# Performance work log

Hardware: AMD Instinct MI355X
Metric: run time of the kernel (lower is better)

Reference implementation:

```python
import jax, jax.numpy as jnp
import numpy as np


def _conv(x, w, b=None, pad=0):
    # x: [B,C,H,W], w: [O,I,kh,kw]
    y = jax.lax.conv_general_dilated(
        x, w, window_strides=(1, 1), padding=[(pad, pad), (pad, pad)],
        dimension_numbers=('NCHW', 'OIHW', 'NCHW'))
    if b is not None:
        y = y + b[None, :, None, None]
    return y


def _resb(x, w1, w2):
    h = _conv(x, w1, pad=1)
    h = jax.nn.leaky_relu(h, 0.1)
    h = _conv(h, w2, pad=1)
    return h + x


def setup_inputs() -> dict:
    key = jax.random.key(0)
    ks = jax.random.split(key, 16)
    B, C, H, W, K = 2, 64, 128, 256, 16
    s = 0.05
    return {
        'x_left': jax.random.normal(ks[0], (B, C, H, W), jnp.float32),
        'x_right': jax.random.normal(ks[1], (B, C, H, W), jnp.float32),
        'xxs': jax.random.randint(ks[2], (B, H * W, K), 0, H, jnp.int32),
        'yys': jax.random.randint(ks[3], (B, H * W, K), 0, W, jnp.int32),
        'is_training': 0,
        'rb_w1': jax.random.normal(ks[4], (C, C, 3, 3), jnp.float32) * s,
        'rb_w2': jax.random.normal(ks[5], (C, C, 3, 3), jnp.float32) * s,
        'b1_w': jax.random.normal(ks[6], (C, C, 1, 1), jnp.float32) * s,
        'b1_b': jax.random.normal(ks[7], (C,), jnp.float32) * s,
        'b2_w': jax.random.normal(ks[8], (C, C, 1, 1), jnp.float32) * s,
        'b2_b': jax.random.normal(ks[9], (C,), jnp.float32) * s,
        'b3_w': jax.random.normal(ks[10], (C, C, 1, 1), jnp.float32) * s,
        'b3_b': jax.random.normal(ks[11], (C,), jnp.float32) * s,
        'fus_w': jax.random.normal(ks[12], (C, 2 * C, 1, 1), jnp.float32) * s,
        'fus_b': jax.random.normal(ks[13], (C,), jnp.float32) * s,
    }


def reference(x_left, x_right, xxs, yys, is_training,
              rb_w1, rb_w2, b1_w, b1_b, b2_w, b2_b, b3_w, b3_b, fus_w, fus_b):
    B, C, H, W = x_left.shape
    HW = H * W
    K = xxs.shape[-1]

    buf_l = _resb(x_left, rb_w1, rb_w2)
    buf_r = _resb(x_right, rb_w1, rb_w2)

    Q = _conv(buf_l, b1_w, b1_b)   # [B,C,H,W]
    S = _conv(buf_r, b2_w, b2_b)
    R = _conv(buf_r, b3_w, b3_b)

    # per-pixel gather: S[b,:,Pos_x,Pos_y] -> flat index into H*W
    flat = (xxs.astype(jnp.int32) * W + yys.astype(jnp.int32)).reshape(B, HW * K)  # [B,HW*K]
    Sf = S.reshape(B, C, HW)
    Rf = R.reshape(B, C, HW)
    Key = jnp.take_along_axis(Sf, flat[:, None, :], axis=2).reshape(B, C, HW, K)
    Val = jnp.take_along_axis(Rf, flat[:, None, :], axis=2).reshape(B, C, HW, K)

    Qv = Q.transpose(0, 2, 3, 1).reshape(B, HW, C)           # [B,HW,C]
    score = jnp.einsum('bpc,bcpk->bpk', Qv, Key)             # [B,HW,K]
    M = jax.nn.softmax(score, axis=-1)                       # [B,HW,K]
    buf = jnp.einsum('bpk,bckp->bpc', M, Val.transpose(0, 1, 3, 2))  # [B,HW,C]
    buf = buf.reshape(B, H, W, C).transpose(0, 3, 1, 2)      # [B,C,H,W]

    out = _conv(jnp.concatenate([buf, x_left], axis=1), fus_w, fus_b)
    M_right_to_left = M[:, :, None, :]                       # [B,HW,1,K] as in torch
    if is_training == 1:
        return out
    return (out, M_right_to_left)
```

## Files before the change

kernel.cpp:

```cpp
#include <hip/hip_runtime.h>

#define HH 128
#define WW 256
#define CH 64
#define HWP (HH * WW)

typedef __attribute__((ext_vector_type(8))) __bf16 bf16x8;
typedef __attribute__((ext_vector_type(16))) float float16;

__device__ __forceinline__ unsigned short f2bf(float f) {
    unsigned u = __float_as_uint(f);
    u += 0x7fffu + ((u >> 16) & 1u);
    return (unsigned short)(u >> 16);
}
__device__ __forceinline__ float bf2f(unsigned short u) {
    return __uint_as_float((unsigned)u << 16);
}

__global__ __launch_bounds__(256) void prep_w_k(
    const float* __restrict__ w1, const float* __restrict__ w2,
    const float* __restrict__ b1w, const float* __restrict__ b2w,
    const float* __restrict__ b3w, const float* __restrict__ fusw,
    unsigned short* __restrict__ wB)
{
    int e = blockIdx.x * 256 + threadIdx.x;
    if (e >= 94208) return;
    float val;
    if (e < 73728) {
        const float* w = (e < 36864) ? w1 : w2;
        int t = (e < 36864) ? e : e - 36864;
        int j = t & 7, L = (t >> 3) & 63, nb = (t >> 9) & 1, kc = t >> 10;
        int k  = kc * 16 + (L >> 5) * 8 + j;
        int n  = nb * 32 + (L & 31);
        int kd = k >> 6, ci = k & 63;
        val = w[(n * 64 + ci) * 9 + kd];
    } else {
        int t = e - 73728;
        if (t < 4096) {
            int j = t & 7, L = (t >> 3) & 63, i3 = t >> 9;
            int nt = i3 & 1, kc = i3 >> 1;
            int n = nt * 32 + (L & 31), k = kc * 16 + (L >> 5) * 8 + j;
            val = b1w[n * 64 + k];
        } else if (t < 12288) {
            t -= 4096;
            int j = t & 7, L = (t >> 3) & 63, i3 = t >> 9;
            int nt = i3 & 3, kc = i3 >> 2;
            int n = nt * 32 + (L & 31), k = kc * 16 + (L >> 5) * 8 + j;
            val = (n < 64) ? b2w[n * 64 + k] : b3w[(n - 64) * 64 + k];
        } else {
            t -= 12288;
            int j = t & 7, L = (t >> 3) & 63, i3 = t >> 9;
            int nt = i3 & 1, kc = i3 >> 1;
            int n = nt * 32 + (L & 31), k = kc * 16 + (L >> 5) * 8 + j;
            val = fusw[n * 128 + k];
        }
    }
    wB[e] = f2bf(val);
}

__global__ __launch_bounds__(256) void toT_k(
    const float* __restrict__ xl, const float* __restrict__ xr,
    unsigned short* __restrict__ XT)
{
    __shared__ __align__(16) unsigned short sT[64 * 68];
    const int tid = threadIdx.x;
    const int side = blockIdx.x >> 10;
    const int i0   = blockIdx.x & 1023;
    const int gp0  = i0 * 64;
    const int b    = gp0 >> 15;
    const int pofs = gp0 & (HWP - 1);
    const float* in = (side ? xr : xl) + (size_t)b * CH * HWP + pofs;

    for (int i = tid; i < 4096; i += 256) {
        int ci = i >> 6, px = i & 63;
        sT[px * 68 + ci] = f2bf(in[(size_t)ci * HWP + px]);
    }
    __syncthreads();
    const int px = tid >> 2, q = tid & 3;
    unsigned short* op = XT + ((size_t)(side * 2 + b) * HWP + pofs + px) * 64;
#pragma unroll
    for (int r = 0; r < 2; ++r)
        *(uint4*)&op[(q * 2 + r) * 8] = *(uint4*)&sT[px * 68 + (q * 2 + r) * 8];
}

__device__ __forceinline__ void stage_halo(
    unsigned short* sA, const unsigned short* inT, int x0, int y, int tid)
{
    for (int i = tid; i < 1584; i += 256) {
        int cell = i >> 3, j = i & 7;
        int row = cell / 66, col = cell - row * 66;
        int gy = y + row - 1, gx = x0 + col - 1;
        uint4 v = make_uint4(0, 0, 0, 0);
        if ((unsigned)gy < HH && (unsigned)gx < WW)
            v = *(const uint4*)&inT[(size_t)(gy * WW + gx) * 64 + j * 8];
        *(uint4*)&sA[(row * 66 + col) * 68 + j * 8] = v;
    }
}

__global__ __launch_bounds__(256) void conv1_k(
    const unsigned short* __restrict__ XT, const unsigned short* __restrict__ wB,
    unsigned short* __restrict__ H1T)
{
    __shared__ __align__(16) unsigned short sA[3 * 66 * 68];

    const int tid = threadIdx.x;
    const int x0  = blockIdx.x * 64;
    const int y   = blockIdx.y;
    const int sb  = blockIdx.z;
    const unsigned short* inT = XT + (size_t)sb * HWP * 64;

    stage_halo(sA, inT, x0, y, tid);
    __syncthreads();

    const int lane = tid & 63, wv = tid >> 6;
    const int mw = wv & 1, nw = wv >> 1;
    const int m = lane & 31, kg = lane >> 5;
    const int px_l = mw * 32 + m;

    float16 acc;
#pragma unroll
    for (int i = 0; i < 16; ++i) acc[i] = 0.f;

#pragma unroll
    for (int kc = 0; kc < 36; ++kc) {
        const int kd = kc >> 2, h = kc & 3;
        const int dy = kd / 3, dx = kd - dy * 3;
        bf16x8 af = *(const bf16x8*)&sA[((dy * 66 + px_l + dx) * 68) + h * 16 + kg * 8];
        bf16x8 bf = *(const bf16x8*)&wB[((kc * 2 + nw) * 64 + lane) * 8];
        acc = __builtin_amdgcn_mfma_f32_32x32x16_bf16(af, bf, acc, 0, 0, 0);
    }

    __syncthreads();
    unsigned short* sCb = sA;
    const int n = nw * 32 + (lane & 31);
#pragma unroll
    for (int r = 0; r < 16; ++r) {
        int pr = mw * 32 + (r & 3) + 8 * (r >> 2) + 4 * kg;
        float v = acc[r];
        v = v > 0.f ? v : 0.1f * v;
        sCb[pr * 68 + n] = f2bf(v);
    }
    __syncthreads();

    const int px = tid >> 2, q = tid & 3;
    unsigned short* op = H1T + ((size_t)sb * HWP + y * WW + x0 + px) * 64;
#pragma unroll
    for (int r = 0; r < 2; ++r)
        *(uint4*)&op[(q * 2 + r) * 8] = *(uint4*)&sCb[px * 68 + (q * 2 + r) * 8];
}

__global__ __launch_bounds__(256) void conv2_k(
    const unsigned short* __restrict__ H1T, const unsigned short* __restrict__ XT,
    const unsigned short* __restrict__ wB2, const unsigned short* __restrict__ wQ,
    const unsigned short* __restrict__ wSR, const float* __restrict__ b1b,
    const float* __restrict__ b2b, const float* __restrict__ b3b,
    unsigned short* __restrict__ QT, unsigned short* __restrict__ ST,
    unsigned short* __restrict__ RT)
{
    __shared__ __align__(16) unsigned short sA[3 * 66 * 68];

    const int tid = threadIdx.x;
    const int x0  = blockIdx.x * 64;
    const int y   = blockIdx.y;
    const int sb  = blockIdx.z;
    const int side = sb >> 1, b = sb & 1;
    const unsigned short* inT = H1T + (size_t)sb * HWP * 64;

    stage_halo(sA, inT, x0, y, tid);
    __syncthreads();

    const int lane = tid & 63, wv = tid >> 6;
    const int mw = wv & 1, nw = wv >> 1;
    const int m = lane & 31, kg = lane >> 5;
    const int px_l = mw * 32 + m;

    float16 acc;
#pragma unroll
    for (int i = 0; i < 16; ++i) acc[i] = 0.f;

#pragma unroll
    for (int kc = 0; kc < 36; ++kc) {
        const int kd = kc >> 2, h = kc & 3;
        const int dy = kd / 3, dx = kd - dy * 3;
        bf16x8 af = *(const bf16x8*)&sA[((dy * 66 + px_l + dx) * 68) + h * 16 + kg * 8];
        bf16x8 bf = *(const bf16x8*)&wB2[((kc * 2 + nw) * 64 + lane) * 8];
        acc = __builtin_amdgcn_mfma_f32_32x32x16_bf16(af, bf, acc, 0, 0, 0);
    }

    __syncthreads();
    unsigned short* sCb = sA;
    unsigned short* sC2 = sA + 4352;
    const int n = nw * 32 + (lane & 31);
    const unsigned short* xres = XT + (size_t)sb * HWP * 64;
#pragma unroll
    for (int r = 0; r < 16; ++r) {
        int pr = mw * 32 + (r & 3) + 8 * (r >> 2) + 4 * kg;
        float xv = bf2f(xres[(size_t)(y * WW + x0 + pr) * 64 + n]);
        sCb[pr * 68 + n] = f2bf(acc[r] + xv);
    }
    __syncthreads();

    if (side == 0) {
        float16 a2;
#pragma unroll
        for (int i = 0; i < 16; ++i) a2[i] = 0.f;
#pragma unroll
        for (int kc = 0; kc < 4; ++kc) {
            bf16x8 af = *(const bf16x8*)&sCb[px_l * 68 + kc * 16 + kg * 8];
            bf16x8 bf = *(const bf16x8*)&wQ[((kc * 2 + nw) * 64 + lane) * 8];
            a2 = __builtin_amdgcn_mfma_f32_32x32x16_bf16(af, bf, a2, 0, 0, 0);
        }
        float bv = b1b[n];
#pragma unroll
        for (int r = 0; r < 16; ++r) {
            int pr = mw * 32 + (r & 3) + 8 * (r >> 2) + 4 * kg;
            sC2[pr * 68 + n] = f2bf(a2[r] + bv);
        }
        __syncthreads();
        const int px = tid >> 2, q = tid & 3;
        unsigned short* op = QT + ((size_t)b * HWP + y * WW + x0 + px) * 64;
#pragma unroll
        for (int r = 0; r < 2; ++r)
            *(uint4*)&op[(q * 2 + r) * 8] = *(uint4*)&sC2[px * 68 + (q * 2 + r) * 8];
    } else {
        float16 a2[2];
#pragma unroll
        for (int t = 0; t < 2; ++t)
#pragma unroll
            for (int i = 0; i < 16; ++i) a2[t][i] = 0.f;
#pragma unroll
        for (int kc = 0; kc < 4; ++kc) {
            bf16x8 af = *(const bf16x8*)&sCb[px_l * 68 + kc * 16 + kg * 8];
#pragma unroll
            for (int t = 0; t < 2; ++t) {
                int nt = nw * 2 + t;
                bf16x8 bf = *(const bf16x8*)&wSR[((kc * 4 + nt) * 64 + lane) * 8];
                a2[t] = __builtin_amdgcn_mfma_f32_32x32x16_bf16(af, bf, a2[t], 0, 0, 0);
            }
        }
#pragma unroll
        for (int t = 0; t < 2; ++t) {
            int nn = (nw * 2 + t) * 32 + (lane & 31);
            float bv = (nn < 64) ? b2b[nn] : b3b[nn - 64];
#pragma unroll
            for (int r = 0; r < 16; ++r) {
                int pr = mw * 32 + (r & 3) + 8 * (r >> 2) + 4 * kg;
                sC2[pr * 132 + nn] = f2bf(a2[t][r] + bv);
            }
        }
        __syncthreads();
        const int px = tid >> 2, q = tid & 3;
        const size_t prow = (size_t)b * HWP + y * WW + x0 + px;
        unsigned short* op = ((q < 2) ? ST : RT) + prow * 64 + (q & 1) * 32;
#pragma unroll
        for (int j = 0; j < 4; ++j)
            *(uint4*)&op[j * 8] = *(uint4*)&sC2[px * 132 + q * 32 + j * 8];
    }
}

__global__ __launch_bounds__(512) void attn_fuse_k(
    const unsigned short* __restrict__ QT, const unsigned short* __restrict__ ST,
    const unsigned short* __restrict__ RT, const int* __restrict__ xxs,
    const int* __restrict__ yys, const unsigned short* __restrict__ XT,
    const unsigned short* __restrict__ wfrag, const float* __restrict__ bias,
    float* __restrict__ out, float* __restrict__ Mout)
{
    __shared__ __align__(16) unsigned char smem[64 * 68 * 4];
    unsigned short* sBuf = (unsigned short*)smem;
    unsigned short* sXT  = (unsigned short*)smem + 64 * 68;
    float*          sC   = (float*)smem;

    const int tid  = threadIdx.x;
    const int lane = tid & 63;
    const int wv   = tid >> 6;

    const int blk = blockIdx.x;
    const int b   = (blk & 4) ? 1 : 0;
    const int sub = (blk >> 3) * 4 + (blk & 3);
    const int pofs = sub * 64;
    const size_t gp0   = (size_t)b * HWP + pofs;
    const size_t bbase = (size_t)b * HWP;

    {
        const unsigned short* xlT = XT + gp0 * 64;
        int px = tid >> 3, j = tid & 7;
        *(uint4*)&sXT[px * 68 + j * 8] = *(const uint4*)&xlT[(size_t)px * 64 + j * 8];
    }

    const int k = lane & 15, cq = lane >> 4;
    for (int it = 0; it < 8; ++it) {
        const int pl = wv * 8 + it;
        const size_t gp = gp0 + pl;

        const int flat = xxs[gp * 16 + k] * WW + yys[gp * 16 + k];

        const unsigned short* srow = ST + (bbase + (size_t)flat) * 64 + cq * 16;
        const unsigned short* qrow = QT + gp * 64 + cq * 16;
        float s = 0.f;
#pragma unroll
        for (int hh = 0; hh < 2; ++hh) {
            uint4 sv = *(const uint4*)(srow + hh * 8);
            uint4 qv = *(const uint4*)(qrow + hh * 8);
            const unsigned* sa = (const unsigned*)&sv;
            const unsigned* qa = (const unsigned*)&qv;
#pragma unroll
            for (int d = 0; d < 4; ++d) {
                s = fmaf(__uint_as_float(sa[d] << 16),
                         __uint_as_float(qa[d] << 16), s);
                s = fmaf(__uint_as_float(sa[d] & 0xffff0000u),
                         __uint_as_float(qa[d] & 0xffff0000u), s);
            }
        }
        s += __shfl_xor(s, 16, 64);
        s += __shfl_xor(s, 32, 64);

        float mx = s;
#pragma unroll
        for (int mm = 1; mm <= 8; mm <<= 1) mx = fmaxf(mx, __shfl_xor(mx, mm, 64));
        const float e = __expf(s - mx);
        float sum = e;
#pragma unroll
        for (int mm = 1; mm <= 8; mm <<= 1) sum += __shfl_xor(sum, mm, 64);
        const float mval = e * (1.f / sum);

        if (lane < 16) Mout[gp * 16 + lane] = mval;

        const unsigned short* rbase = RT + bbase * 64;
        float acc = 0.f;
#pragma unroll
        for (int kk = 0; kk < 16; ++kk) {
            int   fi = __builtin_amdgcn_readlane(flat, kk);
            float mk = __uint_as_float(
                __builtin_amdgcn_readlane(__float_as_uint(mval), kk));
            acc = fmaf(mk, bf2f(rbase[(size_t)fi * 64 + lane]), acc);
        }
        sBuf[pl * 68 + lane] = f2bf(acc);
    }
    __syncthreads();

    float16 facc;
#pragma unroll
    for (int i = 0; i < 16; ++i) facc[i] = 0.f;
    const int mw = wv & 1, nw = (wv >> 1) & 1;
    const int m = lane & 31, kg = lane >> 5;
    const int px_l = mw * 32 + m;

    if (tid < 256) {
#pragma unroll
        for (int kc = 0; kc < 8; ++kc) {
            const unsigned short* asrc = (kc < 4)
                ? &sBuf[px_l * 68 + kc * 16 + kg * 8]
                : &sXT[px_l * 68 + (kc - 4) * 16 + kg * 8];
            bf16x8 af = *(const bf16x8*)asrc;
            bf16x8 bf = *(const bf16x8*)&wfrag[((kc * 2 + nw) * 64 + lane) * 8];
            facc = __builtin_amdgcn_mfma_f32_32x32x16_bf16(af, bf, facc, 0, 0, 0);
        }
    }
    __syncthreads();

    if (tid < 256) {
        const int co_l = nw * 32 + (lane & 31);
#pragma unroll
        for (int r = 0; r < 16; ++r) {
            int pr = mw * 32 + (r & 3) + 8 * (r >> 2) + 4 * kg;
            sC[co_l * 68 + pr] = facc[r];
        }
    }
    __syncthreads();

    if (tid < 256) {
        const int co = tid >> 2, p0 = (tid & 3) * 16;
        const float bv = bias[co];
        float* op = out + ((size_t)b * CH + co) * HWP + pofs + p0;
#pragma unroll
        for (int q = 0; q < 4; ++q) {
            float4 v = *(float4*)&sC[co * 68 + p0 + q * 4];
            v.x += bv; v.y += bv; v.z += bv; v.w += bv;
            *(float4*)&op[q * 4] = v;
        }
    }
}

extern "C" void kernel_launch(void* const* d_in, const int* in_sizes, int n_in,
                              void* d_out, int out_size, void* d_ws, size_t ws_size,
                              hipStream_t stream)
{
    const float* x_left  = (const float*)d_in[0];
    const float* x_right = (const float*)d_in[1];
    const int*   xxs     = (const int*)d_in[2];
    const int*   yys     = (const int*)d_in[3];
    const float* rb_w1   = (const float*)d_in[5];
    const float* rb_w2   = (const float*)d_in[6];
    const float* b1_w    = (const float*)d_in[7];
    const float* b1_b    = (const float*)d_in[8];
    const float* b2_w    = (const float*)d_in[9];
    const float* b2_b    = (const float*)d_in[10];
    const float* b3_w    = (const float*)d_in[11];
    const float* b3_b    = (const float*)d_in[12];
    const float* fus_w   = (const float*)d_in[13];
    const float* fus_b   = (const float*)d_in[14];

    float* out  = (float*)d_out;
    float* Mout = out + (size_t)2 * CH * HWP;

    unsigned short* ws2 = (unsigned short*)d_ws;
    unsigned short* XT   = ws2;
    unsigned short* H1T  = ws2 + 8388608;
    unsigned short* QT   = ws2 + 16777216;
    unsigned short* ST   = ws2 + 20971520;
    unsigned short* RT   = ws2 + 25165824;
    unsigned short* wB   = ws2 + 29360128;

    prep_w_k<<<368, 256, 0, stream>>>(rb_w1, rb_w2, b1_w, b2_w, b3_w, fus_w, wB);
    toT_k<<<2048, 256, 0, stream>>>(x_left, x_right, XT);

    dim3 cgrid(WW / 64, HH, 4), cblk(256);
    conv1_k<<<cgrid, cblk, 0, stream>>>(XT, wB, H1T);
    conv2_k<<<cgrid, cblk, 0, stream>>>(H1T, XT, wB + 36864, wB + 73728,
                                        wB + 77824, b1_b, b2_b, b3_b, QT, ST, RT);

    attn_fuse_k<<<1024, 512, 0, stream>>>(QT, ST, RT, xxs, yys, XT,
                                          wB + 86016, fus_b, out, Mout);
}
```

Before: 196.2 us.

## Compute two output rows per conv1 block and merge prep and transpose kernels

```diff
diff --git a/kernel.cpp b/kernel.cpp
--- a/kernel.cpp
+++ b/kernel.cpp
@@ -17,14 +17,37 @@
     return __uint_as_float((unsigned)u << 16);
 }
 
-__global__ __launch_bounds__(256) void prep_w_k(
+__global__ __launch_bounds__(256) void prep_toT_k(
+    const float* __restrict__ xl, const float* __restrict__ xr,
     const float* __restrict__ w1, const float* __restrict__ w2,
     const float* __restrict__ b1w, const float* __restrict__ b2w,
     const float* __restrict__ b3w, const float* __restrict__ fusw,
-    unsigned short* __restrict__ wB)
-{
-    int e = blockIdx.x * 256 + threadIdx.x;
-    if (e >= 94208) return;
+    unsigned short* __restrict__ XT, unsigned short* __restrict__ wB)
+{
+    const int tid = threadIdx.x;
+    if (blockIdx.x < 2048) {
+        __shared__ __align__(16) unsigned short sT[64 * 68];
+        const int side = blockIdx.x >> 10;
+        const int i0   = blockIdx.x & 1023;
+        const int gp0  = i0 * 64;
+        const int b    = gp0 >> 15;
+        const int pofs = gp0 & (HWP - 1);
+        const float* in = (side ? xr : xl) + (size_t)b * CH * HWP + pofs;
+
+        for (int i = tid; i < 4096; i += 256) {
+            int ci = i >> 6, px = i & 63;
+            sT[px * 68 + ci] = f2bf(in[(size_t)ci * HWP + px]);
+        }
+        __syncthreads();
+        const int px = tid >> 2, q = tid & 3;
+        unsigned short* op = XT + ((size_t)(side * 2 + b) * HWP + pofs + px) * 64;
+#pragma unroll
+        for (int r = 0; r < 2; ++r)
+            *(uint4*)&op[(q * 2 + r) * 8] = *(uint4*)&sT[px * 68 + (q * 2 + r) * 8];
+        return;
+    }
+
+    int e = (blockIdx.x - 2048) * 256 + tid;
     float val;
     if (e < 73728) {
         const float* w = (e < 36864) ? w1 : w2;
@@ -58,31 +81,6 @@
     wB[e] = f2bf(val);
 }
 
-__global__ __launch_bounds__(256) void toT_k(
-    const float* __restrict__ xl, const float* __restrict__ xr,
-    unsigned short* __restrict__ XT)
-{
-    __shared__ __align__(16) unsigned short sT[64 * 68];
-    const int tid = threadIdx.x;
-    const int side = blockIdx.x >> 10;
-    const int i0   = blockIdx.x & 1023;
-    const int gp0  = i0 * 64;
-    const int b    = gp0 >> 15;
-    const int pofs = gp0 & (HWP - 1);
-    const float* in = (side ? xr : xl) + (size_t)b * CH * HWP + pofs;
-
-    for (int i = tid; i < 4096; i += 256) {
-        int ci = i >> 6, px = i & 63;
-        sT[px * 68 + ci] = f2bf(in[(size_t)ci * HWP + px]);
-    }
-    __syncthreads();
-    const int px = tid >> 2, q = tid & 3;
-    unsigned short* op = XT + ((size_t)(side * 2 + b) * HWP + pofs + px) * 64;
-#pragma unroll
-    for (int r = 0; r < 2; ++r)
-        *(uint4*)&op[(q * 2 + r) * 8] = *(uint4*)&sT[px * 68 + (q * 2 + r) * 8];
-}
-
 __device__ __forceinline__ void stage_halo(
     unsigned short* sA, const unsigned short* inT, int x0, int y, int tid)
 {
@@ -101,33 +99,44 @@
     const unsigned short* __restrict__ XT, const unsigned short* __restrict__ wB,
     unsigned short* __restrict__ H1T)
 {
-    __shared__ __align__(16) unsigned short sA[3 * 66 * 68];
+    __shared__ __align__(16) unsigned short sA[4 * 66 * 68];
 
     const int tid = threadIdx.x;
     const int x0  = blockIdx.x * 64;
-    const int y   = blockIdx.y;
+    const int y0  = blockIdx.y * 2;
     const int sb  = blockIdx.z;
     const unsigned short* inT = XT + (size_t)sb * HWP * 64;
 
-    stage_halo(sA, inT, x0, y, tid);
+    for (int i = tid; i < 2112; i += 256) {
+        int cell = i >> 3, j = i & 7;
+        int row = cell / 66, col = cell - row * 66;
+        int gy = y0 + row - 1, gx = x0 + col - 1;
+        uint4 v = make_uint4(0, 0, 0, 0);
+        if ((unsigned)gy < HH && (unsigned)gx < WW)
+            v = *(const uint4*)&inT[(size_t)(gy * WW + gx) * 64 + j * 8];
+        *(uint4*)&sA[(row * 66 + col) * 68 + j * 8] = v;
+    }
     __syncthreads();
 
     const int lane = tid & 63, wv = tid >> 6;
-    const int mw = wv & 1, nw = wv >> 1;
+    const int h = wv & 1, nw = wv >> 1;
     const int m = lane & 31, kg = lane >> 5;
-    const int px_l = mw * 32 + m;
-
-    float16 acc;
-#pragma unroll
-    for (int i = 0; i < 16; ++i) acc[i] = 0.f;
+    const int pxl = h * 32 + m;
+
+    float16 acc0, acc1;
+#pragma unroll
+    for (int i = 0; i < 16; ++i) { acc0[i] = 0.f; acc1[i] = 0.f; }
 
 #pragma unroll
     for (int kc = 0; kc < 36; ++kc) {
-        const int kd = kc >> 2, h = kc & 3;
+        const int kd = kc >> 2, hh = kc & 3;
         const int dy = kd / 3, dx = kd - dy * 3;
-        bf16x8 af = *(const bf16x8*)&sA[((dy * 66 + px_l + dx) * 68) + h * 16 + kg * 8];
-        bf16x8 bf = *(const bf16x8*)&wB[((kc * 2 + nw) * 64 + lane) * 8];
-        acc = __builtin_amdgcn_mfma_f32_32x32x16_bf16(af, bf, acc, 0, 0, 0);
+        bf16x8 bfg = *(const bf16x8*)&wB[((kc * 2 + nw) * 64 + lane) * 8];
+        const int base = (dy * 66 + pxl + dx) * 68 + hh * 16 + kg * 8;
+        bf16x8 af0 = *(const bf16x8*)&sA[base];
+        bf16x8 af1 = *(const bf16x8*)&sA[base + 66 * 68];
+        acc0 = __builtin_amdgcn_mfma_f32_32x32x16_bf16(af0, bfg, acc0, 0, 0, 0);
+        acc1 = __builtin_amdgcn_mfma_f32_32x32x16_bf16(af1, bfg, acc1, 0, 0, 0);
     }
 
     __syncthreads();
@@ -135,18 +144,20 @@
     const int n = nw * 32 + (lane & 31);
 #pragma unroll
     for (int r = 0; r < 16; ++r) {
-        int pr = mw * 32 + (r & 3) + 8 * (r >> 2) + 4 * kg;
-        float v = acc[r];
-        v = v > 0.f ? v : 0.1f * v;
-        sCb[pr * 68 + n] = f2bf(v);
-    }
-    __syncthreads();
-
-    const int px = tid >> 2, q = tid & 3;
-    unsigned short* op = H1T + ((size_t)sb * HWP + y * WW + x0 + px) * 64;
-#pragma unroll
-    for (int r = 0; r < 2; ++r)
-        *(uint4*)&op[(q * 2 + r) * 8] = *(uint4*)&sCb[px * 68 + (q * 2 + r) * 8];
+        int prl = h * 32 + (r & 3) + 8 * (r >> 2) + 4 * kg;
+        float v0 = acc0[r]; v0 = v0 > 0.f ? v0 : 0.1f * v0;
+        float v1 = acc1[r]; v1 = v1 > 0.f ? v1 : 0.1f * v1;
+        sCb[prl * 68 + n] = f2bf(v0);
+        sCb[(64 + prl) * 68 + n] = f2bf(v1);
+    }
+    __syncthreads();
+
+    const int px2 = tid >> 1, q = tid & 1;
+    const int rr = px2 >> 6, px = px2 & 63;
+    unsigned short* op = H1T + ((size_t)sb * HWP + (y0 + rr) * WW + x0 + px) * 64 + q * 32;
+#pragma unroll
+    for (int j = 0; j < 4; ++j)
+        *(uint4*)&op[j * 8] = *(uint4*)&sCb[px2 * 68 + q * 32 + j * 8];
 }
 
 __global__ __launch_bounds__(256) void conv2_k(
@@ -411,13 +422,13 @@
     unsigned short* RT   = ws2 + 25165824;
     unsigned short* wB   = ws2 + 29360128;
 
-    prep_w_k<<<368, 256, 0, stream>>>(rb_w1, rb_w2, b1_w, b2_w, b3_w, fus_w, wB);
-    toT_k<<<2048, 256, 0, stream>>>(x_left, x_right, XT);
-
-    dim3 cgrid(WW / 64, HH, 4), cblk(256);
-    conv1_k<<<cgrid, cblk, 0, stream>>>(XT, wB, H1T);
-    conv2_k<<<cgrid, cblk, 0, stream>>>(H1T, XT, wB + 36864, wB + 73728,
-                                        wB + 77824, b1_b, b2_b, b3_b, QT, ST, RT);
+    prep_toT_k<<<2416, 256, 0, stream>>>(x_left, x_right, rb_w1, rb_w2,
+                                         b1_w, b2_w, b3_w, fus_w, XT, wB);
+
+    conv1_k<<<dim3(4, 64, 4), 256, 0, stream>>>(XT, wB, H1T);
+    conv2_k<<<dim3(4, 128, 4), 256, 0, stream>>>(H1T, XT, wB + 36864, wB + 73728,
+                                                 wB + 77824, b1_b, b2_b, b3_b,
+                                                 QT, ST, RT);
 
     attn_fuse_k<<<1024, 512, 0, stream>>>(QT, ST, RT, xxs, yys, XT,
                                           wB + 86016, fus_b, out, Mout);
```

New measurement: 197.2 us. Within noise of the previous version (+0.5%).
